# Optimization experiments

Hardware: AMD Instinct MI355X
Metric: run time of the kernel (lower is better)

The kernel has to match this reference:

```python
import jax, jax.numpy as jnp
import numpy as np

N = 2048      # number of ROIs
C = 1024      # in_channels == inter_channels
G = 16        # groups
D = C // G    # per-group dim = 64


def _bbox_overlaps(b1, b2):
    # mmdet-1.x IoU with +1 pixel convention; b1:(N,4), b2:(M,4)
    area1 = (b1[:, 2] - b1[:, 0] + 1) * (b1[:, 3] - b1[:, 1] + 1)  # (N,)
    area2 = (b2[:, 2] - b2[:, 0] + 1) * (b2[:, 3] - b2[:, 1] + 1)  # (M,)
    lt = jnp.maximum(b1[:, None, :2], b2[None, :, :2])             # (N,M,2)
    rb = jnp.minimum(b1[:, None, 2:], b2[None, :, 2:])             # (N,M,2)
    wh = jnp.clip(rb - lt + 1, 0)
    inter = wh[..., 0] * wh[..., 1]                                # (N,M)
    return inter / (area1[:, None] + area2[None, :] - inter)


def setup_inputs() -> dict:
    key = jax.random.key(0)
    ks = jax.random.split(key, 9)
    in_x = jax.random.normal(ks[0], (N, C), dtype=jnp.float32)
    # valid boxes: [batch_idx, x1, y1, x2, y2]
    xy = jax.random.uniform(ks[1], (N, 2), minval=0.0, maxval=800.0)
    wh = jax.random.uniform(ks[2], (N, 2), minval=8.0, maxval=200.0)
    rois = jnp.concatenate([jnp.zeros((N, 1)), xy, xy + wh], axis=1).astype(jnp.float32)
    s = 1.0 / np.sqrt(C)
    W0 = jax.random.normal(ks[3], (C, C), dtype=jnp.float32) * s
    b0 = jnp.zeros((C,), dtype=jnp.float32)
    W1 = jax.random.normal(ks[4], (C, C), dtype=jnp.float32) * s
    b1 = jnp.zeros((C,), dtype=jnp.float32)
    # grouped 1x1 conv: per group maps C channels -> D channels
    Wout = jax.random.normal(ks[5], (G, D, C), dtype=jnp.float32) * s
    bout = jnp.zeros((C,), dtype=jnp.float32)
    return {"in_x": in_x, "rois": rois, "W0": W0, "b0": b0, "W1": W1,
            "b1": b1, "Wout": Wout, "bout": bout}


def reference(in_x, rois, W0, b0, W1, b1, Wout, bout):
    # self-attention path: in_ref_x = in_x, ref_rois = rois
    # embed convs are pre-activation (relu -> 1x1 conv), shared for x and ref_x
    def embed(v):
        v = jax.nn.relu(v) @ W0.T + b0
        v = jax.nn.relu(v) @ W1.T + b1
        return v
    x = embed(in_x)                      # (N, C)
    ref_x = x                            # shared convs, same input
    xg = x.reshape(N, G, D)
    rg = ref_x.reshape(N, G, D)
    scores = jnp.einsum('ngd,mgd->ngm', xg, rg) / jnp.sqrt(jnp.float32(D))  # (N,G,N)
    ious = _bbox_overlaps(rois[:, 1:], rois[:, 1:])                          # (N,N)
    scores = scores + jnp.log(ious[:, None, :] + 1e-6)
    attn = jax.nn.softmax(scores, axis=2)                                    # (N,G,N)
    y = jnp.einsum('ngm,mc->ngc', attn, in_x)                                # (N,G,C)
    out = jnp.einsum('ngc,goc->ngo', y, Wout).reshape(N, C) + bout           # (N,C)
    return out
```

## Files before the change

kernel.cpp:

```cpp
#include <hip/hip_runtime.h>
#include <math.h>

constexpr int NROI = 2048;
constexpr int CDIM = 1024;
constexpr int NG   = 16;
constexpr int DH   = 64;

typedef __attribute__((ext_vector_type(8))) short short8;
typedef __attribute__((ext_vector_type(4))) float floatx4;

#define MFMA_BF16(a, b, c) __builtin_amdgcn_mfma_f32_16x16x32_bf16((a), (b), (c), 0, 0, 0)

__device__ __forceinline__ short f2bf(float f) {
  unsigned u = __float_as_uint(f);
  unsigned r = 0x7fffu + ((u >> 16) & 1u);
  return (short)((u + r) >> 16);
}
__device__ __forceinline__ float bf2f(unsigned short u) {
  return __uint_as_float(((unsigned)u) << 16);
}
__device__ __forceinline__ unsigned pack2(float a, float b) {
  return (unsigned)(unsigned short)f2bf(a) | ((unsigned)(unsigned short)f2bf(b) << 16);
}

typedef __attribute__((address_space(1))) void GV;
typedef __attribute__((address_space(3))) void LV;
__device__ __forceinline__ void gl2lds16(const void* g, void* l) {
  __builtin_amdgcn_global_load_lds((GV*)g, (LV*)l, 16, 0, 0);
}

__device__ __forceinline__ short8 brelu(short8 v) {
  union { short8 s; unsigned u[4]; } x; x.s = v;
#pragma unroll
  for (int i = 0; i < 4; ++i) {
    unsigned m = (x.u[i] >> 15) & 0x10001u;
    x.u[i] &= ~(m * 0xFFFFu);
  }
  return x.s;
}

__global__ __launch_bounds__(256) void convert_kernel(
    const float* __restrict__ in_x, const float* __restrict__ W0,
    const float* __restrict__ W1, const float* __restrict__ Wout,
    short* __restrict__ xin_b, short* __restrict__ W0b,
    short* __restrict__ W1b, short* __restrict__ Woutb)
{
  const int i = blockIdx.x * 256 + threadIdx.x;
  {
    const float4 v = ((const float4*)in_x)[i];
    uint2 u; u.x = pack2(v.x, v.y); u.y = pack2(v.z, v.w);
    ((uint2*)xin_b)[i] = u;
  }
  if (i < 262144) {
    float4 v = ((const float4*)W0)[i];
    uint2 u; u.x = pack2(v.x, v.y); u.y = pack2(v.z, v.w);
    ((uint2*)W0b)[i] = u;
    v = ((const float4*)W1)[i];
    u.x = pack2(v.x, v.y); u.y = pack2(v.z, v.w);
    ((uint2*)W1b)[i] = u;
    v = ((const float4*)Wout)[i];
    u.x = pack2(v.x, v.y); u.y = pack2(v.z, v.w);
    ((uint2*)Woutb)[i] = u;
  }
}

__global__ __launch_bounds__(256) void iou4_kernel(const float* __restrict__ rois,
                                                   unsigned short* __restrict__ biasb)
{
  const int q  = blockIdx.y;
  const int k0 = (blockIdx.x * 256 + threadIdx.x) * 4;
  const float qx1 = rois[q * 5 + 1], qy1 = rois[q * 5 + 2];
  const float qx2 = rois[q * 5 + 3], qy2 = rois[q * 5 + 4];
  const float qa = (qx2 - qx1 + 1.f) * (qy2 - qy1 + 1.f);
  float v[4];
#pragma unroll
  for (int j = 0; j < 4; ++j) {
    const int k = k0 + j;
    const float kx1 = rois[k * 5 + 1], ky1 = rois[k * 5 + 2];
    const float kx2 = rois[k * 5 + 3], ky2 = rois[k * 5 + 4];
    const float ka = (kx2 - kx1 + 1.f) * (ky2 - ky1 + 1.f);
    float iw = fminf(qx2, kx2) - fmaxf(qx1, kx1) + 1.f;
    float ih = fminf(qy2, ky2) - fmaxf(qy1, ky1) + 1.f;
    iw = fmaxf(iw, 0.f); ih = fmaxf(ih, 0.f);
    const float inter = iw * ih;
    v[j] = inter * __builtin_amdgcn_rcpf(qa + ka - inter) + 1e-6f;
  }
  uint2 u; u.x = pack2(v[0], v[1]); u.y = pack2(v[2], v[3]);
  *(uint2*)&biasb[(size_t)q * NROI + k0] = u;
}

template <int FUSED>
__global__ __launch_bounds__(256, 4) void gemm64(
    const short* __restrict__ A, const short* __restrict__ Ba,
    const short* __restrict__ Bb, const float* __restrict__ bias,
    short* __restrict__ outRM, short* __restrict__ outTR)
{
  __shared__ short As[2][8 * 512];
  __shared__ short Bs[2][8 * 512];
  const int t = threadIdx.x, w = t >> 6, lane = t & 63;
  const int wm = w >> 1, wn = w & 1;
  const int row0 = blockIdx.y * 64;
  bool isW0; int col0; const short* B;
  if (FUSED) {
    isW0 = blockIdx.x < 16;
    col0 = (blockIdx.x & 15) * 64;
    B = isW0 ? Ba : Bb;
  } else {
    isW0 = true; col0 = blockIdx.x * 64; B = Ba;
  }
  const bool doRelu = FUSED ? isW0 : true;
  const int rlo = lane & 15, khi = (lane >> 4) * 8;

  floatx4 acc[2][2];
#pragma unroll
  for (int i = 0; i < 2; ++i)
#pragma unroll
    for (int j = 0; j < 2; ++j) acc[i][j] = (floatx4){0.f, 0.f, 0.f, 0.f};

#pragma unroll
  for (int kh = 0; kh < 2; ++kh) {
    const int f = w * 2 + kh;
    gl2lds16(A + (size_t)(row0 + w * 16 + rlo) * CDIM + kh * 32 + khi, &As[0][f * 512]);
    gl2lds16(B + (size_t)(col0 + w * 16 + rlo) * CDIM + kh * 32 + khi, &Bs[0][f * 512]);
  }
  __syncthreads();

  for (int it = 0; it < 16; ++it) {
    const int p = it & 1;
    if (it < 15) {
      const int k1 = (it + 1) * 64;
#pragma unroll
      for (int kh = 0; kh < 2; ++kh) {
        const int f = w * 2 + kh;
        gl2lds16(A + (size_t)(row0 + w * 16 + rlo) * CDIM + k1 + kh * 32 + khi,
                 &As[1 - p][f * 512]);
        gl2lds16(B + (size_t)(col0 + w * 16 + rlo) * CDIM + k1 + kh * 32 + khi,
                 &Bs[1 - p][f * 512]);
      }
    }
#pragma unroll
    for (int kh = 0; kh < 2; ++kh) {
      short8 a[2], bf[2];
#pragma unroll
      for (int i = 0; i < 2; ++i) {
        a[i] = *(const short8*)&As[p][((wm * 2 + i) * 2 + kh) * 512 + lane * 8];
        if (doRelu) a[i] = brelu(a[i]);
      }
#pragma unroll
      for (int j = 0; j < 2; ++j)
        bf[j] = *(const short8*)&Bs[p][((wn * 2 + j) * 2 + kh) * 512 + lane * 8];
#pragma unroll
      for (int i = 0; i < 2; ++i)
#pragma unroll
        for (int j = 0; j < 2; ++j)
          acc[i][j] = MFMA_BF16(a[i], bf[j], acc[i][j]);
    }
    __syncthreads();
  }

  const int colL = lane & 15, qq = lane >> 4;
  if (!FUSED || isW0) {
    float bj[2];
    bj[0] = bias[col0 + wn * 32 + colL];
    bj[1] = bias[col0 + wn * 32 + 16 + colL];
#pragma unroll
    for (int i = 0; i < 2; ++i)
#pragma unroll
      for (int j = 0; j < 2; ++j)
#pragma unroll
        for (int r = 0; r < 4; ++r) {
          const int row = row0 + wm * 32 + i * 16 + qq * 4 + r;
          const int cc  = col0 + wn * 32 + j * 16 + colL;
          outRM[(size_t)row * CDIM + cc] = f2bf(acc[i][j][r] + bj[j]);
        }
  } else {
#pragma unroll
    for (int i = 0; i < 2; ++i)
#pragma unroll
      for (int j = 0; j < 2; ++j) {
        unsigned long long u =
            (unsigned long long)pack2(acc[i][j][0], acc[i][j][1]) |
            ((unsigned long long)pack2(acc[i][j][2], acc[i][j][3]) << 32);
        const int cc  = col0 + wn * 32 + j * 16 + colL;
        const int row = row0 + wm * 32 + i * 16 + qq * 4;
        *(unsigned long long*)&outTR[(size_t)cc * NROI + row] = u;
      }
  }
}

__global__ __launch_bounds__(512) void attn_bias(
    const short* __restrict__ Xb,
    const short* __restrict__ ZTb,
    const unsigned short* __restrict__ biasb,
    const float* __restrict__ bout,
    float* __restrict__ Out)
{
  const int g  = blockIdx.y;
  const int n0 = blockIdx.x * 128;
  const int t  = threadIdx.x;
  const int w    = t >> 6;
  const int lane = t & 63;
  const int col  = lane & 15;
  const int qq   = lane >> 4;
  const int t16 = (w >> 1) * 16;
  const int h32 = (w & 1) * 32;
  const int rlo = lane & 15, khi = (lane >> 4) * 8;

  __shared__ short Kf[2][8 * 512];
  __shared__ short Vf[2][8 * 512];
  __shared__ short Pf[8 * 1024];

  const size_t qoff = (size_t)(n0 + w * 16 + col) * CDIM + g * DH;
  const short8 qf0 = *(const short8*)(Xb + qoff + qq * 8);
  const short8 qf1 = *(const short8*)(Xb + qoff + 32 + qq * 8);

  floatx4 oc[4];
#pragma unroll
  for (int dt = 0; dt < 4; ++dt) oc[dt] = (floatx4){0.f, 0.f, 0.f, 0.f};
  float lsum[4] = {0.f, 0.f, 0.f, 0.f};

  gl2lds16(Xb + (size_t)(t16 + rlo) * CDIM + g * DH + h32 + khi, &Kf[0][w * 512]);
  gl2lds16(ZTb + (size_t)(g * DH + t16 + rlo) * NROI + h32 + khi, &Vf[0][w * 512]);
  __syncthreads();

  for (int it = 0; it < NROI / 64; ++it) {
    const int p  = it & 1;
    const int m0 = it * 64;
    if (it + 1 < NROI / 64) {
      const int m1 = m0 + 64;
      gl2lds16(Xb + (size_t)(m1 + t16 + rlo) * CDIM + g * DH + h32 + khi,
               &Kf[1 - p][w * 512]);
      gl2lds16(ZTb + (size_t)(g * DH + t16 + rlo) * NROI + m1 + h32 + khi,
               &Vf[1 - p][w * 512]);
    }

    float bb[4][4];
#pragma unroll
    for (int ct = 0; ct < 4; ++ct)
#pragma unroll
      for (int r = 0; r < 4; ++r)
        bb[ct][r] = bf2f(biasb[(size_t)(n0 + w * 16 + qq * 4 + r) * NROI +
                               m0 + ct * 16 + col]);

    floatx4 sc[4];
#pragma unroll
    for (int ct = 0; ct < 4; ++ct) {
      const short8 b0 = *(const short8*)&Kf[p][(ct * 2 + 0) * 512 + lane * 8];
      const short8 b1 = *(const short8*)&Kf[p][(ct * 2 + 1) * 512 + lane * 8];
      floatx4 z4 = (floatx4){0.f, 0.f, 0.f, 0.f};
      z4 = MFMA_BF16(qf0, b0, z4);
      z4 = MFMA_BF16(qf1, b1, z4);
      sc[ct] = z4;
    }

#pragma unroll
    for (int ct = 0; ct < 4; ++ct)
#pragma unroll
      for (int r = 0; r < 4; ++r)
        sc[ct][r] = __expf(sc[ct][r] * 0.125f) * bb[ct][r];
#pragma unroll
    for (int r = 0; r < 4; ++r)
      lsum[r] += sc[0][r] + sc[1][r] + sc[2][r] + sc[3][r];

    {
      short* pw = &Pf[w * 1024];
#pragma unroll
      for (int ct = 0; ct < 4; ++ct) {
        const int key = ct * 16 + col;
        const int base = (key >> 5) * 512 + (key & 7);
#pragma unroll
        for (int r = 0; r < 4; ++r) {
          const int dl = (4 * qq + r) + ((key >> 3) & 3) * 16;
          pw[base + dl * 8] = f2bf(sc[ct][r]);
        }
      }
      const short8 pa0 = *(const short8*)&pw[0 * 512 + lane * 8];
      const short8 pa1 = *(const short8*)&pw[1 * 512 + lane * 8];
#pragma unroll
      for (int dt = 0; dt < 4; ++dt) {
        const short8 v0 = *(const short8*)&Vf[p][(dt * 2 + 0) * 512 + lane * 8];
        const short8 v1 = *(const short8*)&Vf[p][(dt * 2 + 1) * 512 + lane * 8];
        oc[dt] = MFMA_BF16(pa0, v0, oc[dt]);
        oc[dt] = MFMA_BF16(pa1, v1, oc[dt]);
      }
    }
    __syncthreads();
  }

#pragma unroll
  for (int r = 0; r < 4; ++r) {
    float s = lsum[r];
    s += __shfl_xor(s, 1); s += __shfl_xor(s, 2);
    s += __shfl_xor(s, 4); s += __shfl_xor(s, 8);
    lsum[r] = s;
  }
#pragma unroll
  for (int dt = 0; dt < 4; ++dt) {
    const float bo = bout[g * DH + dt * 16 + col];
#pragma unroll
    for (int r = 0; r < 4; ++r)
      Out[(size_t)(n0 + w * 16 + qq * 4 + r) * CDIM + g * DH + dt * 16 + col] =
          oc[dt][r] / lsum[r] + bo;
  }
}

extern "C" void kernel_launch(void* const* d_in, const int* in_sizes, int n_in,
                              void* d_out, int out_size, void* d_ws, size_t ws_size,
                              hipStream_t stream) {
  const float* in_x = (const float*)d_in[0];
  const float* rois = (const float*)d_in[1];
  const float* W0   = (const float*)d_in[2];
  const float* b0   = (const float*)d_in[3];
  const float* W1   = (const float*)d_in[4];
  const float* b1   = (const float*)d_in[5];
  const float* Wout = (const float*)d_in[6];
  const float* bout = (const float*)d_in[7];
  char* w8 = (char*)d_ws;

  short* xin_b = (short*)w8;
  short* W0b   = (short*)(w8 + ((size_t)4 << 20));
  short* W1b   = (short*)(w8 + ((size_t)6 << 20));
  short* Woutb = (short*)(w8 + ((size_t)8 << 20));
  short* zT    = (short*)(w8 + ((size_t)10 << 20));
  unsigned short* biasb = (unsigned short*)(w8 + ((size_t)14 << 20));
  short* xb  = xin_b;
  short* t0b = (short*)d_out;

  convert_kernel<<<2048, 256, 0, stream>>>(in_x, W0, W1, Wout,
                                           xin_b, W0b, W1b, Woutb);
  iou4_kernel<<<dim3(2, NROI), 256, 0, stream>>>(rois, biasb);
  gemm64<1><<<dim3(32, 32), 256, 0, stream>>>(xin_b, W0b, Woutb, b0, t0b, zT);
  gemm64<0><<<dim3(16, 32), 256, 0, stream>>>(t0b, W1b, nullptr, b1, xb, nullptr);
  attn_bias<<<dim3(NROI / 128, NG), 512, 0, stream>>>(xb, zT, biasb, bout,
                                                      (float*)d_out);
}
```

Measured before the change: 188.9 us.

## Split attention key range across two half-blocks and compute transposed scores in registers

The attention kernel now runs 1024 threads per block. The two halves each process half of the key range, and their partial outputs and row sums are combined through shared memory at the end. Scores are computed as K·Q^T, so each lane already holds the probability fragment in the layout the PV MFMA expects. This removes the LDS round-trip for P. The IoU bias and the V-transpose are written with a permuted key order (keypos) so the loads match this layout, and bias is read as vectorized 16-byte loads instead of scattered scalar loads. The cost is more LDS per block, fewer iterations per wave, and a final cross-half reduction.

```diff
diff --git a/kernel.cpp b/kernel.cpp
--- a/kernel.cpp
+++ b/kernel.cpp
@@ -37,6 +37,10 @@
     x.u[i] &= ~(m * 0xFFFFu);
   }
   return x.s;
+}
+
+__device__ __forceinline__ int keypos(int k) {
+  return (k & ~31) | (((k >> 2) & 3) << 3) | (((k >> 4) & 1) << 2);
 }
 
 __global__ __launch_bounds__(256) void convert_kernel(
@@ -86,7 +90,7 @@
     v[j] = inter * __builtin_amdgcn_rcpf(qa + ka - inter) + 1e-6f;
   }
   uint2 u; u.x = pack2(v[0], v[1]); u.y = pack2(v[2], v[3]);
-  *(uint2*)&biasb[(size_t)q * NROI + k0] = u;
+  *(uint2*)&biasb[(size_t)q * NROI + keypos(k0)] = u;
 }
 
 template <int FUSED>
@@ -183,12 +187,12 @@
             ((unsigned long long)pack2(acc[i][j][2], acc[i][j][3]) << 32);
         const int cc  = col0 + wn * 32 + j * 16 + colL;
         const int row = row0 + wm * 32 + i * 16 + qq * 4;
-        *(unsigned long long*)&outTR[(size_t)cc * NROI + row] = u;
+        *(unsigned long long*)&outTR[(size_t)cc * NROI + keypos(row)] = u;
       }
   }
 }
 
-__global__ __launch_bounds__(512) void attn_bias(
+__global__ __launch_bounds__(1024, 4) void attn_bias(
     const short* __restrict__ Xb,
     const short* __restrict__ ZTb,
     const unsigned short* __restrict__ biasb,
@@ -199,108 +203,122 @@
   const int n0 = blockIdx.x * 128;
   const int t  = threadIdx.x;
   const int w    = t >> 6;
+  const int half = w >> 3;
+  const int wq   = w & 7;
   const int lane = t & 63;
   const int col  = lane & 15;
   const int qq   = lane >> 4;
-  const int t16 = (w >> 1) * 16;
-  const int h32 = (w & 1) * 32;
-  const int rlo = lane & 15, khi = (lane >> 4) * 8;
-
-  __shared__ short Kf[2][8 * 512];
-  __shared__ short Vf[2][8 * 512];
-  __shared__ short Pf[8 * 1024];
-
-  const size_t qoff = (size_t)(n0 + w * 16 + col) * CDIM + g * DH;
+  const int t16 = (wq >> 1) * 16;
+  const int h32 = (wq & 1) * 32;
+  const int rlo = lane & 15, khi = qq * 8;
+
+  __shared__ short Kf[2][2][4096];
+  __shared__ short Vf[2][2][4096];
+
+  const size_t qoff = (size_t)(n0 + wq * 16 + col) * CDIM + g * DH;
   const short8 qf0 = *(const short8*)(Xb + qoff + qq * 8);
   const short8 qf1 = *(const short8*)(Xb + qoff + 32 + qq * 8);
 
   floatx4 oc[4];
 #pragma unroll
   for (int dt = 0; dt < 4; ++dt) oc[dt] = (floatx4){0.f, 0.f, 0.f, 0.f};
-  float lsum[4] = {0.f, 0.f, 0.f, 0.f};
-
-  gl2lds16(Xb + (size_t)(t16 + rlo) * CDIM + g * DH + h32 + khi, &Kf[0][w * 512]);
-  gl2lds16(ZTb + (size_t)(g * DH + t16 + rlo) * NROI + h32 + khi, &Vf[0][w * 512]);
+  float lsum = 0.f;
+
+  const int mbase = half * 1024;
+  gl2lds16(Xb + (size_t)(mbase + t16 + rlo) * CDIM + g * DH + h32 + khi,
+           &Kf[half][0][wq * 512]);
+  gl2lds16(ZTb + (size_t)(g * DH + t16 + rlo) * NROI + mbase + h32 + khi,
+           &Vf[half][0][wq * 512]);
   __syncthreads();
 
-  for (int it = 0; it < NROI / 64; ++it) {
+  const unsigned short* bq =
+      biasb + (size_t)(n0 + wq * 16 + col) * NROI + mbase + qq * 8;
+
+  for (int it = 0; it < 16; ++it) {
     const int p  = it & 1;
-    const int m0 = it * 64;
-    if (it + 1 < NROI / 64) {
+    const int m0 = mbase + it * 64;
+
+    union { short8 s[2]; unsigned short h[16]; } BU;
+    BU.s[0] = *(const short8*)(bq + it * 64);
+    BU.s[1] = *(const short8*)(bq + it * 64 + 32);
+
+    if (it + 1 < 16) {
       const int m1 = m0 + 64;
       gl2lds16(Xb + (size_t)(m1 + t16 + rlo) * CDIM + g * DH + h32 + khi,
-               &Kf[1 - p][w * 512]);
+               &Kf[half][1 - p][wq * 512]);
       gl2lds16(ZTb + (size_t)(g * DH + t16 + rlo) * NROI + m1 + h32 + khi,
-               &Vf[1 - p][w * 512]);
-    }
-
-    float bb[4][4];
+               &Vf[half][1 - p][wq * 512]);
+    }
+
+    float e[4][4];
+#pragma unroll
+    for (int ct = 0; ct < 4; ++ct) {
+      const short8 k0 = *(const short8*)&Kf[half][p][(ct * 2 + 0) * 512 + lane * 8];
+      const short8 k1 = *(const short8*)&Kf[half][p][(ct * 2 + 1) * 512 + lane * 8];
+      floatx4 z4 = (floatx4){0.f, 0.f, 0.f, 0.f};
+      z4 = MFMA_BF16(k0, qf0, z4);
+      z4 = MFMA_BF16(k1, qf1, z4);
+#pragma unroll
+      for (int r = 0; r < 4; ++r) e[ct][r] = z4[r];
+    }
+
 #pragma unroll
     for (int ct = 0; ct < 4; ++ct)
 #pragma unroll
+      for (int r = 0; r < 4; ++r) {
+        const float pv = __expf(e[ct][r] * 0.125f) * bf2f(BU.h[ct * 4 + r]);
+        e[ct][r] = pv;
+        lsum += pv;
+      }
+
+    union { short8 s; unsigned u[4]; } U0, U1;
+#pragma unroll
+    for (int j = 0; j < 2; ++j) {
+      U0.u[j * 2 + 0] = pack2(e[j][0], e[j][1]);
+      U0.u[j * 2 + 1] = pack2(e[j][2], e[j][3]);
+      U1.u[j * 2 + 0] = pack2(e[j + 2][0], e[j + 2][1]);
+      U1.u[j * 2 + 1] = pack2(e[j + 2][2], e[j + 2][3]);
+    }
+
+#pragma unroll
+    for (int dt = 0; dt < 4; ++dt) {
+      const short8 v0 = *(const short8*)&Vf[half][p][(dt * 2 + 0) * 512 + lane * 8];
+      const short8 v1 = *(const short8*)&Vf[half][p][(dt * 2 + 1) * 512 + lane * 8];
+      oc[dt] = MFMA_BF16(U0.s, v0, oc[dt]);
+      oc[dt] = MFMA_BF16(U1.s, v1, oc[dt]);
+    }
+    __syncthreads();
+  }
+
+  float s = lsum;
+  s += __shfl_xor(s, 16);
+  s += __shfl_xor(s, 32);
+
+  float* ocb = (float*)&Kf[0][0][0];
+  float* lsb = (float*)&Vf[0][0][0];
+  const int cbase = (wq * 64 + lane) * 16;
+  if (half) {
+#pragma unroll
+    for (int dt = 0; dt < 4; ++dt)
+#pragma unroll
+      for (int r = 0; r < 4; ++r) ocb[cbase + dt * 4 + r] = oc[dt][r];
+    lsb[wq * 64 + lane] = s;
+  }
+  __syncthreads();
+  if (!half) {
+    s += lsb[wq * 64 + lane];
+    float ls[4];
+#pragma unroll
+    for (int r = 0; r < 4; ++r)
+      ls[r] = __shfl(s, (qq << 4) | (qq * 4 + r));
+#pragma unroll
+    for (int dt = 0; dt < 4; ++dt) {
+      const float bo = bout[g * DH + dt * 16 + col];
+#pragma unroll
       for (int r = 0; r < 4; ++r)
-        bb[ct][r] = bf2f(biasb[(size_t)(n0 + w * 16 + qq * 4 + r) * NROI +
-                               m0 + ct * 16 + col]);
-
-    floatx4 sc[4];
-#pragma unroll
-    for (int ct = 0; ct < 4; ++ct) {
-      const short8 b0 = *(const short8*)&Kf[p][(ct * 2 + 0) * 512 + lane * 8];
-      const short8 b1 = *(const short8*)&Kf[p][(ct * 2 + 1) * 512 + lane * 8];
-      floatx4 z4 = (floatx4){0.f, 0.f, 0.f, 0.f};
-      z4 = MFMA_BF16(qf0, b0, z4);
-      z4 = MFMA_BF16(qf1, b1, z4);
-      sc[ct] = z4;
-    }
-
-#pragma unroll
-    for (int ct = 0; ct < 4; ++ct)
-#pragma unroll
-      for (int r = 0; r < 4; ++r)
-        sc[ct][r] = __expf(sc[ct][r] * 0.125f) * bb[ct][r];
-#pragma unroll
-    for (int r = 0; r < 4; ++r)
-      lsum[r] += sc[0][r] + sc[1][r] + sc[2][r] + sc[3][r];
-
-    {
-      short* pw = &Pf[w * 1024];
-#pragma unroll
-      for (int ct = 0; ct < 4; ++ct) {
-        const int key = ct * 16 + col;
-        const int base = (key >> 5) * 512 + (key & 7);
-#pragma unroll
-        for (int r = 0; r < 4; ++r) {
-          const int dl = (4 * qq + r) + ((key >> 3) & 3) * 16;
-          pw[base + dl * 8] = f2bf(sc[ct][r]);
-        }
-      }
-      const short8 pa0 = *(const short8*)&pw[0 * 512 + lane * 8];
-      const short8 pa1 = *(const short8*)&pw[1 * 512 + lane * 8];
-#pragma unroll
-      for (int dt = 0; dt < 4; ++dt) {
-        const short8 v0 = *(const short8*)&Vf[p][(dt * 2 + 0) * 512 + lane * 8];
-        const short8 v1 = *(const short8*)&Vf[p][(dt * 2 + 1) * 512 + lane * 8];
-        oc[dt] = MFMA_BF16(pa0, v0, oc[dt]);
-        oc[dt] = MFMA_BF16(pa1, v1, oc[dt]);
-      }
-    }
-    __syncthreads();
-  }
-
-#pragma unroll
-  for (int r = 0; r < 4; ++r) {
-    float s = lsum[r];
-    s += __shfl_xor(s, 1); s += __shfl_xor(s, 2);
-    s += __shfl_xor(s, 4); s += __shfl_xor(s, 8);
-    lsum[r] = s;
-  }
-#pragma unroll
-  for (int dt = 0; dt < 4; ++dt) {
-    const float bo = bout[g * DH + dt * 16 + col];
-#pragma unroll
-    for (int r = 0; r < 4; ++r)
-      Out[(size_t)(n0 + w * 16 + qq * 4 + r) * CDIM + g * DH + dt * 16 + col] =
-          oc[dt][r] / lsum[r] + bo;
+        Out[(size_t)(n0 + wq * 16 + qq * 4 + r) * CDIM + g * DH + dt * 16 + col] =
+            (oc[dt][r] + ocb[cbase + dt * 4 + r]) / ls[r] + bo;
+    }
   }
 }
 
@@ -331,6 +349,6 @@
   iou4_kernel<<<dim3(2, NROI), 256, 0, stream>>>(rois, biasb);
   gemm64<1><<<dim3(32, 32), 256, 0, stream>>>(xin_b, W0b, Woutb, b0, t0b, zT);
   gemm64<0><<<dim3(16, 32), 256, 0, stream>>>(t0b, W1b, nullptr, b1, xb, nullptr);
-  attn_bias<<<dim3(NROI / 128, NG), 512, 0, stream>>>(xb, zT, biasb, bout,
-                                                      (float*)d_out);
-}
+  attn_bias<<<dim3(NROI / 128, NG), 1024, 0, stream>>>(xb, zT, biasb, bout,
+                                                       (float*)d_out);
+}
```

Result: faster. 183.9 us (-2.6%).
